# Kernel tuning notes

Hardware: AMD Instinct MI355X
Metric: run time of the kernel (lower is better)

The kernel has to match this reference:

```python
import jax, jax.numpy as jnp
import numpy as np
import math

B, C, T = 4, 512, 2048
H = 8            # num_heads
G = 32           # GroupNorm groups (GroupNorm32 in ADM-style code)
EPS = 1e-5


def setup_inputs() -> dict:
    key = jax.random.key(0)
    ks = jax.random.split(key, 7)
    x = jax.random.normal(ks[0], (B, C, T), jnp.float32)
    norm_scale = 1.0 + 0.02 * jax.random.normal(ks[1], (C,), jnp.float32)
    norm_bias = 0.02 * jax.random.normal(ks[2], (C,), jnp.float32)
    qkv_w = 0.02 * jax.random.normal(ks[3], (3 * C, C), jnp.float32)  # 1x1 conv == matmul
    qkv_b = 0.02 * jax.random.normal(ks[4], (3 * C,), jnp.float32)
    proj_w = 0.02 * jax.random.normal(ks[5], (C, C), jnp.float32)
    proj_b = 0.02 * jax.random.normal(ks[6], (C,), jnp.float32)
    return {"x": x, "norm_scale": norm_scale, "norm_bias": norm_bias,
            "qkv_w": qkv_w, "qkv_b": qkv_b, "proj_w": proj_w, "proj_b": proj_b}


def _group_norm(x, scale, bias):
    # x: [B, C, T]; 32-group norm over (C/G, T) per group
    b, c, t = x.shape
    xg = x.reshape(b, G, (c // G) * t)
    mean = jnp.mean(xg, axis=-1, keepdims=True)
    var = jnp.var(xg, axis=-1, keepdims=True)
    xg = (xg - mean) * jax.lax.rsqrt(var + EPS)
    return xg.reshape(b, c, t) * scale[None, :, None] + bias[None, :, None]


def reference(x, norm_scale, norm_bias, qkv_w, qkv_b, proj_w, proj_b):
    b, c, t = x.shape
    ch = c // H
    h = _group_norm(x, norm_scale, norm_bias)
    qkv = jnp.einsum('oc,bct->bot', qkv_w, h) + qkv_b[None, :, None]  # [B, 3C, T]
    q, k, v = jnp.split(qkv, 3, axis=1)
    q = q.reshape(b * H, ch, t)
    k = k.reshape(b * H, ch, t)
    v = v.reshape(b * H, ch, t)
    scale = 1.0 / math.sqrt(math.sqrt(ch))
    w = jnp.einsum('bct,bcs->bts', q * scale, k * scale)              # [B*H, T, T]
    w = jax.nn.softmax(w.astype(jnp.float32), axis=-1).astype(qkv.dtype)
    a = jnp.einsum('bts,bcs->bct', w, v).reshape(b, c, t)             # [B, C, T]
    out = jnp.einsum('oc,bct->bot', proj_w, a) + proj_b[None, :, None]
    return x + out
```

## Files before the change

kernel.cpp:

```cpp
#include <hip/hip_runtime.h>

typedef short bf16x8 __attribute__((ext_vector_type(8)));
typedef float f32x4 __attribute__((ext_vector_type(4)));
typedef float f32x16 __attribute__((ext_vector_type(16)));
typedef unsigned short u16;
typedef unsigned int u32;

constexpr int B = 4, C = 512, T = 2048, H = 8, G = 32;
constexpr int CH = C / H;
constexpr int CPG = C / G;
constexpr float EPS = 1e-5f;
constexpr float SCLQ = 0.18033688011112042f;

__device__ __forceinline__ u16 f2bf(float f) {
  union { float f; u32 u; } v; v.f = f;
  return (u16)((v.u + 0x7FFFu + ((v.u >> 16) & 1u)) >> 16);
}

__device__ __forceinline__ void gload16(const void* g, void* lds) {
  __builtin_amdgcn_global_load_lds(
      (const __attribute__((address_space(1))) void*)g,
      (__attribute__((address_space(3))) void*)lds, 16, 0, 0);
}

__device__ __forceinline__ void pl32swap(u32& a, u32& b) {
  asm("v_permlane32_swap_b32 %0, %1" : "+v"(a), "+v"(b));
}

template <int ROWS>
__device__ __forceinline__ void stage_swz_4w(u16* lds, const u16* gsrc, int ldk) {
  const int tid = threadIdx.x;
  const int w = tid >> 6, lane = tid & 63;
#pragma unroll
  for (int i = 0; i < ROWS / 32; ++i) {
    const int chunk = i * 4 + w;
    const int row = chunk * 8 + (lane >> 3);
    const int col = ((lane & 7) * 8) ^ ((row & 7) << 3);
    gload16(gsrc + (size_t)row * ldk + col, (char*)lds + chunk * 1024);
  }
}

template <int ROWS>
__device__ __forceinline__ void stage_swz_8w(u16* lds, const u16* gsrc, int ldk) {
  const int tid = threadIdx.x;
  const int w = tid >> 6, lane = tid & 63;
#pragma unroll
  for (int i = 0; i < ROWS / 64; ++i) {
    const int chunk = i * 8 + w;
    const int row = chunk * 8 + (lane >> 3);
    const int col = ((lane & 7) * 8) ^ ((row & 7) << 3);
    gload16(gsrc + (size_t)row * ldk + col, (char*)lds + chunk * 1024);
  }
}

__global__ __launch_bounds__(256) void prep_k(const float* __restrict__ x,
                                              float* __restrict__ stats,
                                              const float* __restrict__ s1,
                                              u16* __restrict__ d1, int n1,
                                              const float* __restrict__ s2,
                                              u16* __restrict__ d2, int n2) {
  __shared__ float red[8];
  const int bid = blockIdx.x;
  if (bid < 1024) {
    int i = bid * 256 + threadIdx.x;
    const float4* src = (const float4*)s1;
    uint2* dst = (uint2*)d1;
    if (i >= n1) { i -= n1; if (i >= n2) return; src = (const float4*)s2; dst = (uint2*)d2; }
    float4 v = src[i];
    uint2 pk;
    pk.x = (u32)f2bf(v.x) | ((u32)f2bf(v.y) << 16);
    pk.y = (u32)f2bf(v.z) | ((u32)f2bf(v.w) << 16);
    dst[i] = pk;
    return;
  }
  const int bg = bid - 1024;
  const float4* xp = (const float4*)(x + (size_t)bg * CPG * T);
  float s = 0.f, ss = 0.f;
  for (int i = threadIdx.x; i < CPG * T / 4; i += 256) {
    float4 v = xp[i];
    s += v.x + v.y + v.z + v.w;
    ss += v.x * v.x + v.y * v.y + v.z * v.z + v.w * v.w;
  }
  for (int off = 32; off; off >>= 1) {
    s += __shfl_down(s, off);
    ss += __shfl_down(ss, off);
  }
  const int w = threadIdx.x >> 6;
  if ((threadIdx.x & 63) == 0) { red[w] = s; red[4 + w] = ss; }
  __syncthreads();
  if (threadIdx.x == 0) {
    float S = red[0] + red[1] + red[2] + red[3];
    float SS = red[4] + red[5] + red[6] + red[7];
    const float inv = 1.f / (float)(CPG * T);
    float mean = S * inv;
    float var = SS * inv - mean * mean;
    stats[bg * 2] = mean;
    stats[bg * 2 + 1] = rsqrtf(var + EPS);
  }
}

__global__ __launch_bounds__(256) void gn_apply_k(const float* __restrict__ x,
                                                  const float* __restrict__ stats,
                                                  const float* __restrict__ gsc,
                                                  const float* __restrict__ gbi,
                                                  u16* __restrict__ ht) {
  const int b = blockIdx.y;
  const int t0 = blockIdx.x * 32;
#pragma unroll
  for (int p = 0; p < 2; ++p) {
    const int c = p * 256 + threadIdx.x;
    const int bg = b * G + (c >> 4);
    const float mean = stats[bg * 2], rstd = stats[bg * 2 + 1];
    const float sc = gsc[c] * rstd;
    const float bi = gbi[c] - mean * sc;
    const float4* xp = (const float4*)(x + ((size_t)b * C + c) * T + t0);
#pragma unroll
    for (int j = 0; j < 8; ++j) {
      float4 v = xp[j];
      const int t = t0 + j * 4;
      u16* hp = ht + ((size_t)b * T + t) * C + c;
      hp[0]     = f2bf(v.x * sc + bi);
      hp[C]     = f2bf(v.y * sc + bi);
      hp[2 * C] = f2bf(v.z * sc + bi);
      hp[3 * C] = f2bf(v.w * sc + bi);
    }
  }
}

__global__ __launch_bounds__(512, 2) void qkv_gemm_k(const u16* __restrict__ ht,
                                                     const u16* __restrict__ wq,
                                                     const float* __restrict__ qkvb,
                                                     u16* __restrict__ qo,
                                                     u16* __restrict__ kvo_k,
                                                     u16* __restrict__ kvo_v) {
  __shared__ u16 As[128 * 64];
  __shared__ u16 Bs[128 * 64];
  const int bid = blockIdx.x;
  const int wg = (bid & 7) * 96 + (bid >> 3);
  const int nt = wg % 12;
  const int mtb = wg / 12;
  const int mt = mtb & 15, b = mtb >> 4;
  const u16* Ab = ht + ((size_t)b * T + mt * 128) * C;
  const u16* Bb = wq + (size_t)nt * 128 * C;
  const int tid = threadIdx.x, lane = tid & 63, w = tid >> 6;
  const int wr = w >> 1, wc = w & 1, l15 = lane & 15, lhi = lane >> 4;
  const int swz = (l15 & 7) << 3;

  const f32x4 vzero = {0.f, 0.f, 0.f, 0.f};
  f32x4 acc[2][4];
#pragma unroll
  for (int m = 0; m < 2; ++m)
#pragma unroll
    for (int n = 0; n < 4; ++n) acc[m][n] = vzero;

  for (int kt = 0; kt < C / 64; ++kt) {
    stage_swz_8w<128>(As, Ab + kt * 64, C);
    stage_swz_8w<128>(Bs, Bb + kt * 64, C);
    __syncthreads();
#pragma unroll
    for (int kk = 0; kk < 2; ++kk) {
      const int koff = (kk * 32 + lhi * 8) ^ swz;
      bf16x8 af[2], bfv[4];
#pragma unroll
      for (int m = 0; m < 2; ++m)
        af[m] = *(const bf16x8*)&As[(wr * 32 + m * 16 + l15) * 64 + koff];
#pragma unroll
      for (int n = 0; n < 4; ++n)
        bfv[n] = *(const bf16x8*)&Bs[(wc * 64 + n * 16 + l15) * 64 + koff];
#pragma unroll
      for (int m = 0; m < 2; ++m)
#pragma unroll
        for (int n = 0; n < 4; ++n)
          acc[m][n] = __builtin_amdgcn_mfma_f32_16x16x32_bf16(af[m], bfv[n], acc[m][n], 0, 0, 0);
    }
    __syncthreads();
  }
#pragma unroll
  for (int n = 0; n < 4; ++n) {
    const int o = nt * 128 + wc * 64 + n * 16 + l15;
    const float bias = qkvb[o];
    const int which = o >> 9, rem = o & 511, hh = rem >> 6, d = rem & 63;
    const size_t bh = (size_t)b * H + hh;
#pragma unroll
    for (int m = 0; m < 2; ++m) {
      const int tbase = mt * 128 + wr * 32 + m * 16 + lhi * 4;
#pragma unroll
      for (int r = 0; r < 4; ++r) {
        float val = acc[m][n][r] + bias;
        if (which == 0) val *= SCLQ;
        const u16 bv = f2bf(val);
        const int t = tbase + r;
        if (which == 0)      qo[(bh * T + t) * CH + d] = bv;
        else if (which == 1) kvo_k[(bh * T + t) * CH + d] = bv;
        else                 kvo_v[(bh * CH + d) * T + t] = bv;
      }
    }
  }
}

__global__ __launch_bounds__(512, 4) void attn_k(const u16* __restrict__ q,
                                                 const u16* __restrict__ k,
                                                 const u16* __restrict__ v,
                                                 u16* __restrict__ at) {
  __shared__ u16 Ks[2][128 * 64];
  __shared__ u16 Vs[2][2][64 * 64];
  const int lin = blockIdx.x + (blockIdx.y << 4);
  const int wg = (lin & 7) * 64 + (lin >> 3);
  const int qt = wg & 15, bh = wg >> 4;
  const int tid = threadIdx.x, lane = tid & 63, w = tid >> 6;
  const int qset = w & 3, grp = w >> 2;
  const int l31 = lane & 31, h = lane >> 5;
  const u16* qb = q + (size_t)bh * T * CH;
  const u16* kb = k + (size_t)bh * T * CH;
  const u16* vb = v + (size_t)bh * CH * T;
  constexpr int NP = T / 128;

  bf16x8 qf[4];
  {
    const u16* qp = qb + (size_t)(qt * 128 + qset * 32 + l31) * CH + h * 8;
#pragma unroll
    for (int ks = 0; ks < 4; ++ks) qf[ks] = *(const bf16x8*)(qp + ks * 16);
  }
  union { u32 u[4]; bf16x8 v8; } ones;
#pragma unroll
  for (int i = 0; i < 4; ++i) ones.u[i] = 0x3F803F80u;

  stage_swz_8w<128>(Ks[0], kb, CH);
  stage_swz_8w<64>(Vs[0][0], vb, T);
  stage_swz_8w<64>(Vs[0][1], vb + 64, T);
  asm volatile("s_waitcnt vmcnt(0)" ::: "memory");
  __builtin_amdgcn_s_barrier();
  asm volatile("" ::: "memory");

  f32x16 accO0 = {0.f,0.f,0.f,0.f,0.f,0.f,0.f,0.f,0.f,0.f,0.f,0.f,0.f,0.f,0.f,0.f};
  f32x16 accO1 = accO0;
  f32x16 accL = accO0;
  const int kswz = (l31 & 7) << 3;

  int cur = 0;
  for (int p = 0; p < NP; ++p) {
    if (p + 1 < NP) {
      stage_swz_8w<128>(Ks[cur ^ 1], kb + (size_t)(p + 1) * 128 * CH, CH);
      stage_swz_8w<64>(Vs[cur ^ 1][0], vb + (p + 1) * 128, T);
      stage_swz_8w<64>(Vs[cur ^ 1][1], vb + (p + 1) * 128 + 64, T);
    }
    const u16* Kc = &Ks[cur][grp * 64 * 64];
    const u16* Vc = Vs[cur][grp];

    f32x16 accS0 = {0.f,0.f,0.f,0.f,0.f,0.f,0.f,0.f,0.f,0.f,0.f,0.f,0.f,0.f,0.f,0.f};
    f32x16 accS1 = accS0;
    __builtin_amdgcn_s_setprio(1);
#pragma unroll
    for (int ks = 0; ks < 4; ++ks) {
      const int col = (ks * 16 + h * 8) ^ kswz;
      bf16x8 kf0 = *(const bf16x8*)&Kc[l31 * 64 + col];
      bf16x8 kf1 = *(const bf16x8*)&Kc[(32 + l31) * 64 + col];
      accS0 = __builtin_amdgcn_mfma_f32_32x32x16_bf16(kf0, qf[ks], accS0, 0, 0, 0);
      accS1 = __builtin_amdgcn_mfma_f32_32x32x16_bf16(kf1, qf[ks], accS1, 0, 0, 0);
    }
    __builtin_amdgcn_s_setprio(0);

    u32 wd0[8], wd1[8];
#pragma unroll
    for (int i = 0; i < 8; ++i) {
      float pa = __builtin_amdgcn_exp2f(accS0[2 * i]);
      float pb = __builtin_amdgcn_exp2f(accS0[2 * i + 1]);
      asm("v_cvt_pk_bf16_f32 %0, %1, %2" : "=v"(wd0[i]) : "v"(pa), "v"(pb));
    }
#pragma unroll
    for (int i = 0; i < 8; ++i) {
      float pa = __builtin_amdgcn_exp2f(accS1[2 * i]);
      float pb = __builtin_amdgcn_exp2f(accS1[2 * i + 1]);
      asm("v_cvt_pk_bf16_f32 %0, %1, %2" : "=v"(wd1[i]) : "v"(pa), "v"(pb));
    }
    pl32swap(wd0[0], wd0[2]); pl32swap(wd0[1], wd0[3]);
    pl32swap(wd0[4], wd0[6]); pl32swap(wd0[5], wd0[7]);
    pl32swap(wd1[0], wd1[2]); pl32swap(wd1[1], wd1[3]);
    pl32swap(wd1[4], wd1[6]); pl32swap(wd1[5], wd1[7]);

    __builtin_amdgcn_s_setprio(1);
#pragma unroll
    for (int kt = 0; kt < 2; ++kt) {
      const u32* wd = kt ? wd1 : wd0;
      union { u32 u[4]; bf16x8 v8; } fa, fb;
      fa.u[0] = wd[0]; fa.u[1] = wd[1]; fa.u[2] = wd[2]; fa.u[3] = wd[3];
      fb.u[0] = wd[4]; fb.u[1] = wd[5]; fb.u[2] = wd[6]; fb.u[3] = wd[7];
      const int sA = (kt * 32 + h * 8) ^ kswz;
      const int sB = (kt * 32 + 16 + h * 8) ^ kswz;
      {
        bf16x8 vf0 = *(const bf16x8*)&Vc[l31 * 64 + sA];
        bf16x8 vf1 = *(const bf16x8*)&Vc[l31 * 64 + sB];
        accO0 = __builtin_amdgcn_mfma_f32_32x32x16_bf16(fa.v8, vf0, accO0, 0, 0, 0);
        accO0 = __builtin_amdgcn_mfma_f32_32x32x16_bf16(fb.v8, vf1, accO0, 0, 0, 0);
      }
      {
        bf16x8 vf0 = *(const bf16x8*)&Vc[(32 + l31) * 64 + sA];
        bf16x8 vf1 = *(const bf16x8*)&Vc[(32 + l31) * 64 + sB];
        accO1 = __builtin_amdgcn_mfma_f32_32x32x16_bf16(fa.v8, vf0, accO1, 0, 0, 0);
        accO1 = __builtin_amdgcn_mfma_f32_32x32x16_bf16(fb.v8, vf1, accO1, 0, 0, 0);
      }
      accL = __builtin_amdgcn_mfma_f32_32x32x16_bf16(fa.v8, ones.v8, accL, 0, 0, 0);
      accL = __builtin_amdgcn_mfma_f32_32x32x16_bf16(fb.v8, ones.v8, accL, 0, 0, 0);
    }
    __builtin_amdgcn_s_setprio(0);

    asm volatile("s_waitcnt vmcnt(0)" ::: "memory");
    __builtin_amdgcn_s_barrier();
    asm volatile("" ::: "memory");
    cur ^= 1;
  }

  float* fO = (float*)&Ks[0][0];
  float* fL = (float*)&Vs[0][0][0];
  if (grp == 1) {
#pragma unroll
    for (int r = 0; r < 16; ++r) {
      const int qrow = (r & 3) + 8 * (r >> 2) + 4 * h;
      float* row = fO + (qset * 32 + qrow) * 64;
      row[l31] = accO0[r];
      row[32 + l31] = accO1[r];
      if (l31 == 0) fL[qset * 32 + qrow] = accL[r];
    }
  }
  __syncthreads();
  if (grp == 0) {
    const int bq = bh >> 3, hh = bh & 7;
#pragma unroll
    for (int r = 0; r < 16; ++r) {
      const int qrow = (r & 3) + 8 * (r >> 2) + 4 * h;
      const float denom = accL[r] + fL[qset * 32 + qrow];
      const float invr = __builtin_amdgcn_rcpf(denom);
      const float* row = fO + (qset * 32 + qrow) * 64;
      const float o0 = accO0[r] + row[l31];
      const float o1 = accO1[r] + row[32 + l31];
      const int t = qt * 128 + qset * 32 + qrow;
      u16* op = at + ((size_t)bq * T + t) * C + hh * 64 + l31;
      op[0]  = f2bf(o0 * invr);
      op[32] = f2bf(o1 * invr);
    }
  }
}

__global__ __launch_bounds__(512, 2) void proj_gemm_k(const u16* __restrict__ at,
                                                      const u16* __restrict__ wp,
                                                      const float* __restrict__ pb,
                                                      const float* __restrict__ x,
                                                      float* __restrict__ out) {
  __shared__ u16 As[128 * 64];
  __shared__ u16 Bs[64 * 64];
  const int bid = blockIdx.x;
  const int wg = (bid & 7) * 64 + (bid >> 3);
  const int nt = wg & 7;
  const int mtb = wg >> 3;
  const int mt = mtb & 15, b = mtb >> 4;
  const u16* Ab = at + ((size_t)b * T + mt * 128) * C;
  const u16* Bb = wp + (size_t)nt * 64 * C;
  const int tid = threadIdx.x, lane = tid & 63, w = tid >> 6;
  const int l15 = lane & 15, lhi = lane >> 4;
  const int swz = (l15 & 7) << 3;

  const f32x4 vzero = {0.f, 0.f, 0.f, 0.f};
  f32x4 acc[4];
#pragma unroll
  for (int n = 0; n < 4; ++n) acc[n] = vzero;

  for (int kt = 0; kt < C / 64; ++kt) {
    stage_swz_8w<128>(As, Ab + kt * 64, C);
    stage_swz_8w<64>(Bs, Bb + kt * 64, C);
    __syncthreads();
#pragma unroll
    for (int kk = 0; kk < 2; ++kk) {
      const int koff = (kk * 32 + lhi * 8) ^ swz;
      bf16x8 af = *(const bf16x8*)&As[(w * 16 + l15) * 64 + koff];
      bf16x8 bfv[4];
#pragma unroll
      for (int n = 0; n < 4; ++n)
        bfv[n] = *(const bf16x8*)&Bs[(n * 16 + l15) * 64 + koff];
#pragma unroll
      for (int n = 0; n < 4; ++n)
        acc[n] = __builtin_amdgcn_mfma_f32_16x16x32_bf16(af, bfv[n], acc[n], 0, 0, 0);
    }
    __syncthreads();
  }
#pragma unroll
  for (int n = 0; n < 4; ++n) {
    const int o = nt * 64 + n * 16 + l15;
    const float bias = pb[o];
    const int tbase = mt * 128 + w * 16 + lhi * 4;
#pragma unroll
    for (int r = 0; r < 4; ++r) {
      const int t = tbase + r;
      const size_t idx = ((size_t)b * C + o) * T + t;
      out[idx] = x[idx] + acc[n][r] + bias;
    }
  }
}

extern "C" void kernel_launch(void* const* d_in, const int* in_sizes, int n_in,
                              void* d_out, int out_size, void* d_ws, size_t ws_size,
                              hipStream_t stream) {
  const float* x     = (const float*)d_in[0];
  const float* gsc   = (const float*)d_in[1];
  const float* gbi   = (const float*)d_in[2];
  const float* qkvw  = (const float*)d_in[3];
  const float* qkvb  = (const float*)d_in[4];
  const float* projw = (const float*)d_in[5];
  const float* projb = (const float*)d_in[6];
  float* out = (float*)d_out;

  char* ws = (char*)d_ws;
  float* stats = (float*)ws;
  u16* wq = (u16*)(ws + 1024);
  u16* wp = (u16*)(ws + 1024 + 1572864);
  u16* ht = (u16*)(ws + 2098176);
  u16* qo = (u16*)(ws + 10486784);
  u16* ko = (u16*)(ws + 18875392);
  u16* vo = (u16*)(ws + 27264000);
  u16* at = ht;

  prep_k<<<1152, 256, 0, stream>>>(x, stats, qkvw, wq, 196608, projw, wp, 65536);
  gn_apply_k<<<dim3(T / 32, B), 256, 0, stream>>>(x, stats, gsc, gbi, ht);
  qkv_gemm_k<<<768, 512, 0, stream>>>(ht, wq, qkvb, qo, ko, vo);
  attn_k<<<dim3(T / 128, B * H), 512, 0, stream>>>(qo, ko, vo, at);
  proj_gemm_k<<<512, 512, 0, stream>>>(at, wp, projb, x, out);
}
```

Measured before the change: 114.1 us.

## Double-buffer GEMM LDS staging, vectorize epilogues, reorder prep blocks, halve GN tile

The QKV and projection GEMMs now double-buffer their LDS tiles, so the next K-slice loads while MFMAs run on the current one, with a single wait and barrier per iteration. The epilogues use packed bf16 conversion (v_cvt_pk_bf16_f32) with an 8-byte store for V, and float4 load/store for the residual add in the projection. prep_k schedules the group-stats blocks first, and gn_apply_k handles 16 timesteps per block instead of 32, doubling its grid. Double buffering doubles LDS per block and may reduce occupancy.

```diff
diff --git a/kernel.cpp b/kernel.cpp
--- a/kernel.cpp
+++ b/kernel.cpp
@@ -17,6 +17,12 @@
   return (u16)((v.u + 0x7FFFu + ((v.u >> 16) & 1u)) >> 16);
 }
 
+__device__ __forceinline__ u32 cvtpk(float lo, float hi) {
+  u32 r;
+  asm("v_cvt_pk_bf16_f32 %0, %1, %2" : "=v"(r) : "v"(lo), "v"(hi));
+  return r;
+}
+
 __device__ __forceinline__ void gload16(const void* g, void* lds) {
   __builtin_amdgcn_global_load_lds(
       (const __attribute__((address_space(1))) void*)g,
@@ -25,19 +31,6 @@
 
 __device__ __forceinline__ void pl32swap(u32& a, u32& b) {
   asm("v_permlane32_swap_b32 %0, %1" : "+v"(a), "+v"(b));
-}
-
-template <int ROWS>
-__device__ __forceinline__ void stage_swz_4w(u16* lds, const u16* gsrc, int ldk) {
-  const int tid = threadIdx.x;
-  const int w = tid >> 6, lane = tid & 63;
-#pragma unroll
-  for (int i = 0; i < ROWS / 32; ++i) {
-    const int chunk = i * 4 + w;
-    const int row = chunk * 8 + (lane >> 3);
-    const int col = ((lane & 7) * 8) ^ ((row & 7) << 3);
-    gload16(gsrc + (size_t)row * ldk + col, (char*)lds + chunk * 1024);
-  }
 }
 
 template <int ROWS>
@@ -61,19 +54,19 @@
                                               u16* __restrict__ d2, int n2) {
   __shared__ float red[8];
   const int bid = blockIdx.x;
-  if (bid < 1024) {
-    int i = bid * 256 + threadIdx.x;
+  if (bid >= 128) {
+    int i = (bid - 128) * 256 + threadIdx.x;
     const float4* src = (const float4*)s1;
     uint2* dst = (uint2*)d1;
     if (i >= n1) { i -= n1; if (i >= n2) return; src = (const float4*)s2; dst = (uint2*)d2; }
     float4 v = src[i];
     uint2 pk;
-    pk.x = (u32)f2bf(v.x) | ((u32)f2bf(v.y) << 16);
-    pk.y = (u32)f2bf(v.z) | ((u32)f2bf(v.w) << 16);
+    pk.x = cvtpk(v.x, v.y);
+    pk.y = cvtpk(v.z, v.w);
     dst[i] = pk;
     return;
   }
-  const int bg = bid - 1024;
+  const int bg = bid;
   const float4* xp = (const float4*)(x + (size_t)bg * CPG * T);
   float s = 0.f, ss = 0.f;
   for (int i = threadIdx.x; i < CPG * T / 4; i += 256) {
@@ -105,7 +98,7 @@
                                                   const float* __restrict__ gbi,
                                                   u16* __restrict__ ht) {
   const int b = blockIdx.y;
-  const int t0 = blockIdx.x * 32;
+  const int t0 = blockIdx.x * 16;
 #pragma unroll
   for (int p = 0; p < 2; ++p) {
     const int c = p * 256 + threadIdx.x;
@@ -115,7 +108,7 @@
     const float bi = gbi[c] - mean * sc;
     const float4* xp = (const float4*)(x + ((size_t)b * C + c) * T + t0);
 #pragma unroll
-    for (int j = 0; j < 8; ++j) {
+    for (int j = 0; j < 4; ++j) {
       float4 v = xp[j];
       const int t = t0 + j * 4;
       u16* hp = ht + ((size_t)b * T + t) * C + c;
@@ -133,8 +126,8 @@
                                                      u16* __restrict__ qo,
                                                      u16* __restrict__ kvo_k,
                                                      u16* __restrict__ kvo_v) {
-  __shared__ u16 As[128 * 64];
-  __shared__ u16 Bs[128 * 64];
+  __shared__ u16 As[2][128 * 64];
+  __shared__ u16 Bs[2][128 * 64];
   const int bid = blockIdx.x;
   const int wg = (bid & 7) * 96 + (bid >> 3);
   const int nt = wg % 12;
@@ -145,6 +138,7 @@
   const int tid = threadIdx.x, lane = tid & 63, w = tid >> 6;
   const int wr = w >> 1, wc = w & 1, l15 = lane & 15, lhi = lane >> 4;
   const int swz = (l15 & 7) << 3;
+  constexpr int NK = C / 64;
 
   const f32x4 vzero = {0.f, 0.f, 0.f, 0.f};
   f32x4 acc[2][4];
@@ -153,27 +147,40 @@
 #pragma unroll
     for (int n = 0; n < 4; ++n) acc[m][n] = vzero;
 
-  for (int kt = 0; kt < C / 64; ++kt) {
-    stage_swz_8w<128>(As, Ab + kt * 64, C);
-    stage_swz_8w<128>(Bs, Bb + kt * 64, C);
-    __syncthreads();
+  stage_swz_8w<128>(As[0], Ab, C);
+  stage_swz_8w<128>(Bs[0], Bb, C);
+  asm volatile("s_waitcnt vmcnt(0)" ::: "memory");
+  __builtin_amdgcn_s_barrier();
+  asm volatile("" ::: "memory");
+
+  int cur = 0;
+  for (int kt = 0; kt < NK; ++kt) {
+    if (kt + 1 < NK) {
+      stage_swz_8w<128>(As[cur ^ 1], Ab + (kt + 1) * 64, C);
+      stage_swz_8w<128>(Bs[cur ^ 1], Bb + (kt + 1) * 64, C);
+    }
 #pragma unroll
     for (int kk = 0; kk < 2; ++kk) {
       const int koff = (kk * 32 + lhi * 8) ^ swz;
       bf16x8 af[2], bfv[4];
 #pragma unroll
       for (int m = 0; m < 2; ++m)
-        af[m] = *(const bf16x8*)&As[(wr * 32 + m * 16 + l15) * 64 + koff];
+        af[m] = *(const bf16x8*)&As[cur][(wr * 32 + m * 16 + l15) * 64 + koff];
 #pragma unroll
       for (int n = 0; n < 4; ++n)
-        bfv[n] = *(const bf16x8*)&Bs[(wc * 64 + n * 16 + l15) * 64 + koff];
+        bfv[n] = *(const bf16x8*)&Bs[cur][(wc * 64 + n * 16 + l15) * 64 + koff];
 #pragma unroll
       for (int m = 0; m < 2; ++m)
 #pragma unroll
         for (int n = 0; n < 4; ++n)
           acc[m][n] = __builtin_amdgcn_mfma_f32_16x16x32_bf16(af[m], bfv[n], acc[m][n], 0, 0, 0);
     }
-    __syncthreads();
+    if (kt + 1 < NK) {
+      asm volatile("s_waitcnt vmcnt(0)" ::: "memory");
+      __builtin_amdgcn_s_barrier();
+      asm volatile("" ::: "memory");
+    }
+    cur ^= 1;
   }
 #pragma unroll
   for (int n = 0; n < 4; ++n) {
@@ -184,15 +191,19 @@
 #pragma unroll
     for (int m = 0; m < 2; ++m) {
       const int tbase = mt * 128 + wr * 32 + m * 16 + lhi * 4;
-#pragma unroll
-      for (int r = 0; r < 4; ++r) {
-        float val = acc[m][n][r] + bias;
-        if (which == 0) val *= SCLQ;
-        const u16 bv = f2bf(val);
-        const int t = tbase + r;
-        if (which == 0)      qo[(bh * T + t) * CH + d] = bv;
-        else if (which == 1) kvo_k[(bh * T + t) * CH + d] = bv;
-        else                 kvo_v[(bh * CH + d) * T + t] = bv;
+      float v0 = acc[m][n][0] + bias, v1 = acc[m][n][1] + bias;
+      float v2 = acc[m][n][2] + bias, v3 = acc[m][n][3] + bias;
+      if (which == 0) { v0 *= SCLQ; v1 *= SCLQ; v2 *= SCLQ; v3 *= SCLQ; }
+      const u32 w01 = cvtpk(v0, v1), w23 = cvtpk(v2, v3);
+      if (which == 2) {
+        uint2 pk; pk.x = w01; pk.y = w23;
+        *(uint2*)&kvo_v[(bh * CH + d) * T + tbase] = pk;
+      } else {
+        u16* dst = (which == 0) ? qo : kvo_k;
+        dst[(bh * T + tbase) * CH + d]     = (u16)(w01 & 0xffff);
+        dst[(bh * T + tbase + 1) * CH + d] = (u16)(w01 >> 16);
+        dst[(bh * T + tbase + 2) * CH + d] = (u16)(w23 & 0xffff);
+        dst[(bh * T + tbase + 3) * CH + d] = (u16)(w23 >> 16);
       }
     }
   }
@@ -346,8 +357,8 @@
                                                       const float* __restrict__ pb,
                                                       const float* __restrict__ x,
                                                       float* __restrict__ out) {
-  __shared__ u16 As[128 * 64];
-  __shared__ u16 Bs[64 * 64];
+  __shared__ u16 As[2][128 * 64];
+  __shared__ u16 Bs[2][64 * 64];
   const int bid = blockIdx.x;
   const int wg = (bid & 7) * 64 + (bid >> 3);
   const int nt = wg & 7;
@@ -358,41 +369,57 @@
   const int tid = threadIdx.x, lane = tid & 63, w = tid >> 6;
   const int l15 = lane & 15, lhi = lane >> 4;
   const int swz = (l15 & 7) << 3;
+  constexpr int NK = C / 64;
 
   const f32x4 vzero = {0.f, 0.f, 0.f, 0.f};
   f32x4 acc[4];
 #pragma unroll
   for (int n = 0; n < 4; ++n) acc[n] = vzero;
 
-  for (int kt = 0; kt < C / 64; ++kt) {
-    stage_swz_8w<128>(As, Ab + kt * 64, C);
-    stage_swz_8w<64>(Bs, Bb + kt * 64, C);
-    __syncthreads();
+  stage_swz_8w<128>(As[0], Ab, C);
+  stage_swz_8w<64>(Bs[0], Bb, C);
+  asm volatile("s_waitcnt vmcnt(0)" ::: "memory");
+  __builtin_amdgcn_s_barrier();
+  asm volatile("" ::: "memory");
+
+  int cur = 0;
+  for (int kt = 0; kt < NK; ++kt) {
+    if (kt + 1 < NK) {
+      stage_swz_8w<128>(As[cur ^ 1], Ab + (kt + 1) * 64, C);
+      stage_swz_8w<64>(Bs[cur ^ 1], Bb + (kt + 1) * 64, C);
+    }
 #pragma unroll
     for (int kk = 0; kk < 2; ++kk) {
       const int koff = (kk * 32 + lhi * 8) ^ swz;
-      bf16x8 af = *(const bf16x8*)&As[(w * 16 + l15) * 64 + koff];
+      bf16x8 af = *(const bf16x8*)&As[cur][(w * 16 + l15) * 64 + koff];
       bf16x8 bfv[4];
 #pragma unroll
       for (int n = 0; n < 4; ++n)
-        bfv[n] = *(const bf16x8*)&Bs[(n * 16 + l15) * 64 + koff];
+        bfv[n] = *(const bf16x8*)&Bs[cur][(n * 16 + l15) * 64 + koff];
 #pragma unroll
       for (int n = 0; n < 4; ++n)
         acc[n] = __builtin_amdgcn_mfma_f32_16x16x32_bf16(af, bfv[n], acc[n], 0, 0, 0);
     }
-    __syncthreads();
+    if (kt + 1 < NK) {
+      asm volatile("s_waitcnt vmcnt(0)" ::: "memory");
+      __builtin_amdgcn_s_barrier();
+      asm volatile("" ::: "memory");
+    }
+    cur ^= 1;
   }
 #pragma unroll
   for (int n = 0; n < 4; ++n) {
     const int o = nt * 64 + n * 16 + l15;
     const float bias = pb[o];
     const int tbase = mt * 128 + w * 16 + lhi * 4;
-#pragma unroll
-    for (int r = 0; r < 4; ++r) {
-      const int t = tbase + r;
-      const size_t idx = ((size_t)b * C + o) * T + t;
-      out[idx] = x[idx] + acc[n][r] + bias;
-    }
+    const size_t idx = ((size_t)b * C + o) * T + tbase;
+    const float4 xv = *(const float4*)&x[idx];
+    float4 ov;
+    ov.x = xv.x + acc[n][0] + bias;
+    ov.y = xv.y + acc[n][1] + bias;
+    ov.z = xv.z + acc[n][2] + bias;
+    ov.w = xv.w + acc[n][3] + bias;
+    *(float4*)&out[idx] = ov;
   }
 }
 
@@ -419,7 +446,7 @@
   u16* at = ht;
 
   prep_k<<<1152, 256, 0, stream>>>(x, stats, qkvw, wq, 196608, projw, wp, 65536);
-  gn_apply_k<<<dim3(T / 32, B), 256, 0, stream>>>(x, stats, gsc, gbi, ht);
+  gn_apply_k<<<dim3(T / 16, B), 256, 0, stream>>>(x, stats, gsc, gbi, ht);
   qkv_gemm_k<<<768, 512, 0, stream>>>(ht, wq, qkvb, qo, ko, vo);
   attn_k<<<dim3(T / 128, B * H), 512, 0, stream>>>(qo, ko, vo, at);
   proj_gemm_k<<<512, 512, 0, stream>>>(at, wp, projb, x, out);
```

After: 104.4 us. -8.5%, faster.
